# Kernel tuning notes

Hardware: AMD Instinct MI355X
Metric: run time of the kernel (lower is better)

Reference implementation:

```python
import jax, jax.numpy as jnp
import numpy as np

DS, TS = 2048, 4096          # drug_size, target_size
N = DS + TS                  # total nodes; also feature dim of x
E = 1048576                  # number of directed edges
NEG_SLOPE = 0.2              # PyG GATConv default negative_slope
GAMMA = 2.0 ** -5            # h1..h4 gamma
PS = [1.0, 0.5, 0.333, 0.25, 0.2]  # drug_ps == target_ps kernel weights


def _segment_softmax(logits, seg, n):
    # softmax over edges grouped by destination node (variable degree)
    m = jax.ops.segment_max(logits, seg, num_segments=n)
    m = jnp.where(jnp.isfinite(m), m, 0.0)
    e = jnp.exp(logits - m[seg])
    s = jax.ops.segment_sum(e, seg, num_segments=n)
    return e / s[seg]


def _gat(h, src, dst, W, a_src, a_dst, b, n):
    # PyG GATConv: linear -> per-edge attention logits -> segment softmax -> scatter-sum, concat heads
    Hh, F = a_src.shape
    z = (h @ W).reshape(n, Hh, F)          # [N, H, F]
    zs = z[src]                            # gather: [E, H, F]
    logit = jnp.einsum('ehf,hf->eh', zs, a_src) + jnp.einsum('ehf,hf->eh', z[dst], a_dst)
    alpha = _segment_softmax(jax.nn.leaky_relu(logit, NEG_SLOPE), dst, n)  # [E, H]
    out = jax.ops.segment_sum(alpha[:, :, None] * zs, dst, num_segments=n)  # scatter: [N, H, F]
    return out.reshape(n, Hh * F) + b


def _gip(y, gamma):
    # getGipKernel(y, 0, gamma, True): row min-max normalize, gram, scale by mean diag, gaussian of distance
    mn = y.min(axis=1, keepdims=True)
    mx = y.max(axis=1, keepdims=True)
    rng = mx - mn
    y = (y - mn) / jnp.where(rng == 0, 1.0, rng)
    k = y @ y.T
    k = k / jnp.mean(jnp.diagonal(k))
    d = jnp.diagonal(k)
    dist = d[:, None] + d[None, :] - 2.0 * k   # kernelToDistance
    return jnp.exp(-gamma * dist)


def _norm_kernel(K):
    # normalized_kernel: abs, replace zeros with min nonzero, divide by diag (D*D.T with 1-D D == diag(K))
    K = jnp.abs(K)
    minv = jnp.min(jnp.where(K == 0, jnp.inf, K))
    K = jnp.where(K == 0, minv, K)
    return K / jnp.diagonal(K)[None, :]


def setup_inputs() -> dict:
    key = jax.random.key(0)
    ks = jax.random.split(key, 24)

    def w(k, shape, fan_in):
        return jax.random.normal(k, shape, jnp.float32) / np.float32(np.sqrt(fan_in))

    return dict(
        x=jax.random.normal(ks[0], (N, N), jnp.float32),
        edge_index=jax.random.randint(ks[1], (2, E), 0, N, dtype=jnp.int32),
        W1=w(ks[2], (N, 256), N), a_src1=w(ks[3], (4, 64), 64), a_dst1=w(ks[4], (4, 64), 64), b1=jnp.zeros((256,), jnp.float32),
        W2=w(ks[5], (256, 256), 256), a_src2=w(ks[6], (4, 64), 64), a_dst2=w(ks[7], (4, 64), 64), b2=jnp.zeros((256,), jnp.float32),
        W3=w(ks[8], (256, 256), 256), a_src3=w(ks[9], (4, 64), 64), a_dst3=w(ks[10], (4, 64), 64), b3=jnp.zeros((256,), jnp.float32),
        W4=w(ks[11], (256, 128), 256), a_src4=w(ks[12], (4, 32), 32), a_dst4=w(ks[13], (4, 32), 32), b4=jnp.zeros((128,), jnp.float32),
        alpha1=jax.random.normal(ks[14], (DS, TS), jnp.float32),
        alpha2=jax.random.normal(ks[15], (TS, DS), jnp.float32),
        drug_sim=jax.random.uniform(ks[16], (DS, DS), jnp.float32),
        target_sim=jax.random.uniform(ks[17], (TS, TS), jnp.float32),
    )


def reference(x, edge_index, W1, a_src1, a_dst1, b1, W2, a_src2, a_dst2, b2,
              W3, a_src3, a_dst3, b3, W4, a_src4, a_dst4, b4,
              alpha1, alpha2, drug_sim, target_sim):
    n = x.shape[0]
    loop = jnp.arange(n, dtype=edge_index.dtype)   # GATConv add_self_loops=True
    src = jnp.concatenate([edge_index[0], loop])
    dst = jnp.concatenate([edge_index[1], loop])

    H1 = jax.nn.relu(_gat(x, src, dst, W1, a_src1, a_dst1, b1, n))
    H2 = jax.nn.relu(_gat(H1, src, dst, W2, a_src2, a_dst2, b2, n))
    H3 = jax.nn.relu(_gat(H2, src, dst, W3, a_src3, a_dst3, b3, n))
    H4 = jax.nn.relu(_gat(H3, src, dst, W4, a_src4, a_dst4, b4, n))

    dks = [_gip(H[:DS], GAMMA) for H in (H1, H2, H3, H4)] + [drug_sim]
    tks = [_gip(H[DS:], GAMMA) for H in (H1, H2, H3, H4)] + [target_sim]
    drug_k = sum(PS[i] * dks[i] for i in range(5))
    target_k = sum(PS[i] * tks[i] for i in range(5))
    drug_k = _norm_kernel(drug_k)
    target_k = _norm_kernel(target_k)

    out = (drug_k @ alpha1 + (target_k @ alpha2).T) / 2.0   # [DS, TS]
    return out
```

## Files before the change

kernel.cpp:

```cpp
#include <hip/hip_runtime.h>
#include <math.h>

#define NN 6144
#define DSZ 2048
#define TSZ 4096
#define NE 1048576
#define NE_TOT (NE + NN)
#define NEG_SLOPE 0.2f
#define GGAMMA 0.03125f

typedef float floatx4 __attribute__((ext_vector_type(4)));
typedef __bf16 bf16x8 __attribute__((ext_vector_type(8)));

__global__ void hist_kernel(const int* __restrict__ ei, int* __restrict__ cnt) {
    int e = blockIdx.x * blockDim.x + threadIdx.x;
    if (e >= NE_TOT) return;
    int d = (e < NE) ? ei[NE + e] : (e - NE);
    atomicAdd(&cnt[d], 1);
}

__global__ void scan_kernel(const int* __restrict__ cnt, int* __restrict__ row_ofs) {
    __shared__ int part[1024];
    int t = threadIdx.x;
    int local[6];
    int s = 0;
#pragma unroll
    for (int i = 0; i < 6; i++) { local[i] = s; s += cnt[t * 6 + i]; }
    part[t] = s;
    __syncthreads();
    for (int off = 1; off < 1024; off <<= 1) {
        int v = (t >= off) ? part[t - off] : 0;
        __syncthreads();
        part[t] += v;
        __syncthreads();
    }
    int base = (t == 0) ? 0 : part[t - 1];
#pragma unroll
    for (int i = 0; i < 6; i++) row_ofs[t * 6 + i] = base + local[i];
    if (t == 1023) row_ofs[NN] = part[1023];
}

__global__ void copy_cursor(const int* __restrict__ row_ofs, int* __restrict__ cursor) {
    int i = blockIdx.x * blockDim.x + threadIdx.x;
    if (i < NN) cursor[i] = row_ofs[i];
}

__global__ void scatter_kernel(const int* __restrict__ ei, int* __restrict__ cursor,
                               int* __restrict__ col) {
    int e = blockIdx.x * blockDim.x + threadIdx.x;
    if (e >= NE_TOT) return;
    int s, d;
    if (e < NE) { s = ei[e]; d = ei[NE + e]; } else { s = e - NE; d = s; }
    int pos = atomicAdd(&cursor[d], 1);
    col[pos] = s;
}

template <bool ATOMIC>
__global__ __launch_bounds__(256) void gemm64(const float* __restrict__ A,
                                              const float* __restrict__ B,
                                              float* __restrict__ C,
                                              int M, int N, int K) {
    __shared__ float As[16][68];
    __shared__ float Bs[16][68];
    const int tid = threadIdx.x;
    const int tn = tid & 15, tm = tid >> 4;
    const int bm = blockIdx.y * 64, bn = blockIdx.x * 64;
    const int ar = tid >> 2, ac = (tid & 3) * 4;
    const int br = tid >> 4, bc = (tid & 15) * 4;
    int kbeg = 0, kend = K;
    if constexpr (ATOMIC) {
        int klen = K / gridDim.z;
        kbeg = blockIdx.z * klen;
        kend = kbeg + klen;
    }
    const float* Ap = A + (size_t)(bm + ar) * K + ac;
    const float* Bp = B + (size_t)br * N + bn + bc;
    float acc[4][4] = {};
    for (int k0 = kbeg; k0 < kend; k0 += 16) {
        float4 av = *(const float4*)(Ap + k0);
        float4 bv = *(const float4*)(Bp + (size_t)k0 * N);
        As[ac + 0][ar] = av.x; As[ac + 1][ar] = av.y;
        As[ac + 2][ar] = av.z; As[ac + 3][ar] = av.w;
        *(float4*)&Bs[br][bc] = bv;
        __syncthreads();
#pragma unroll
        for (int k = 0; k < 16; k++) {
            float4 a4 = *(const float4*)&As[k][tm * 4];
            float4 b4 = *(const float4*)&Bs[k][tn * 4];
            float aa[4] = {a4.x, a4.y, a4.z, a4.w};
            float bb[4] = {b4.x, b4.y, b4.z, b4.w};
#pragma unroll
            for (int i = 0; i < 4; i++)
#pragma unroll
                for (int j = 0; j < 4; j++) acc[i][j] = fmaf(aa[i], bb[j], acc[i][j]);
        }
        __syncthreads();
    }
#pragma unroll
    for (int i = 0; i < 4; i++) {
        float* cp = C + (size_t)(bm + tm * 4 + i) * N + bn + tn * 4;
        if constexpr (ATOMIC) {
#pragma unroll
            for (int j = 0; j < 4; j++) atomicAdd(cp + j, acc[i][j]);
        } else {
            *(float4*)cp = make_float4(acc[i][0], acc[i][1], acc[i][2], acc[i][3]);
        }
    }
}

__device__ __forceinline__ ushort bf16_rne(float x) {
    unsigned u = __float_as_uint(x);
    unsigned r = (u + 0x7fffu + ((u >> 16) & 1u)) >> 16;
    return (ushort)r;
}

__global__ void split_rm(const float* __restrict__ in, ushort* __restrict__ hi,
                         ushort* __restrict__ lo, size_t n4) {
    for (size_t i = (size_t)blockIdx.x * blockDim.x + threadIdx.x; i < n4;
         i += (size_t)gridDim.x * blockDim.x) {
        float4 v = ((const float4*)in)[i];
        float vv[4] = {v.x, v.y, v.z, v.w};
        ushort h[4], l[4];
#pragma unroll
        for (int j = 0; j < 4; j++) {
            h[j] = bf16_rne(vv[j]);
            float hf = __uint_as_float((unsigned)h[j] << 16);
            l[j] = bf16_rne(vv[j] - hf);
        }
        ((ushort4*)hi)[i] = make_ushort4(h[0], h[1], h[2], h[3]);
        ((ushort4*)lo)[i] = make_ushort4(l[0], l[1], l[2], l[3]);
    }
}

__global__ void split_T(const float* __restrict__ in, ushort* __restrict__ hiT,
                        ushort* __restrict__ loT, int R, int C) {
    __shared__ float tile[32][33];
    int bx = blockIdx.x * 32, by = blockIdx.y * 32;
    int tx = threadIdx.x & 31, ty = threadIdx.x >> 5;
#pragma unroll
    for (int k = 0; k < 32; k += 8)
        tile[ty + k][tx] = in[(size_t)(by + ty + k) * C + bx + tx];
    __syncthreads();
#pragma unroll
    for (int k = 0; k < 32; k += 8) {
        float v = tile[tx][ty + k];
        ushort h = bf16_rne(v);
        float hf = __uint_as_float((unsigned)h << 16);
        ushort l = bf16_rne(v - hf);
        size_t o = (size_t)(bx + ty + k) * R + by + tx;
        hiT[o] = h;
        loT[o] = l;
    }
}

__device__ __forceinline__ void gl_lds16(const void* g, void* l) {
    __builtin_amdgcn_global_load_lds(
        (const __attribute__((address_space(1))) unsigned int*)g,
        (__attribute__((address_space(3))) unsigned int*)l, 16, 0, 0);
}

template <int EPI>
__global__ __launch_bounds__(256) void gemm_bt_x3(
    const ushort* __restrict__ Ah, const ushort* __restrict__ Al,
    const ushort* __restrict__ Bh, const ushort* __restrict__ Bl,
    float* __restrict__ C, int M, int N, int K,
    const float* __restrict__ rbuf, const float* __restrict__ md0buf, float p) {
    __shared__ ushort lds[4][4096];
    const int t = threadIdx.x;
    const int bm = blockIdx.y * 128, bn = blockIdx.x * 128;

    const int srow = t >> 2;
    const int scb = (t & 3) << 4;
    const int gcb = scb ^ (((srow >> 1) & 3) << 4);
    const int wid = t >> 6, lane = t & 63;

    const ushort* srcs[4] = {Ah, Al, Bh, Bl};
    const char* g[8];
    ushort* lp[8];
#pragma unroll
    for (int b = 0; b < 4; b++) {
        int rb = (b < 2) ? bm : bn;
#pragma unroll
        for (int i = 0; i < 2; i++) {
            g[b * 2 + i] = (const char*)srcs[b] + ((size_t)(rb + i * 64 + srow) * K) * 2 + gcb;
            lp[b * 2 + i] = &lds[b][i * 2048 + wid * 512];
        }
    }

    floatx4 acc[4][4];
#pragma unroll
    for (int m = 0; m < 4; m++)
#pragma unroll
        for (int n = 0; n < 4; n++) acc[m][n] = (floatx4){0.f, 0.f, 0.f, 0.f};

    const int wr = (wid >> 1) << 6, wc = (wid & 1) << 6;
    const int fr = lane & 15, kh = lane >> 4;
    const int cbf = (((kh << 4) ^ (((fr >> 1) & 3) << 4)) >> 1);

    for (int k0 = 0; k0 < K; k0 += 32) {
#pragma unroll
        for (int q = 0; q < 8; q++) gl_lds16(g[q] + (size_t)k0 * 2, lp[q]);
        __syncthreads();
        bf16x8 bhf[4], blf[4];
#pragma unroll
        for (int n = 0; n < 4; n++) {
            int r = wc + n * 16 + fr;
            bhf[n] = *(const bf16x8*)&lds[2][r * 32 + cbf];
            blf[n] = *(const bf16x8*)&lds[3][r * 32 + cbf];
        }
#pragma unroll
        for (int m = 0; m < 4; m++) {
            int r = wr + m * 16 + fr;
            bf16x8 ahf = *(const bf16x8*)&lds[0][r * 32 + cbf];
            bf16x8 alf = *(const bf16x8*)&lds[1][r * 32 + cbf];
#pragma unroll
            for (int n = 0; n < 4; n++) {
                acc[m][n] = __builtin_amdgcn_mfma_f32_16x16x32_bf16(ahf, bhf[n], acc[m][n], 0, 0, 0);
                acc[m][n] = __builtin_amdgcn_mfma_f32_16x16x32_bf16(ahf, blf[n], acc[m][n], 0, 0, 0);
                acc[m][n] = __builtin_amdgcn_mfma_f32_16x16x32_bf16(alf, bhf[n], acc[m][n], 0, 0, 0);
            }
        }
        __syncthreads();
    }

    float sc = 0.f;
    if constexpr (EPI == 1) sc = GGAMMA / md0buf[0];
#pragma unroll
    for (int m = 0; m < 4; m++) {
#pragma unroll
        for (int n = 0; n < 4; n++) {
#pragma unroll
            for (int r = 0; r < 4; r++) {
                int gr = bm + wr + m * 16 + kh * 4 + r;
                int gc = bn + wc + n * 16 + fr;
                size_t idx = (size_t)gr * N + gc;
                if constexpr (EPI == 0) {
                    C[idx] = acc[m][n][r];
                } else {
                    float val = p * expf(-(rbuf[gr] + rbuf[gc] - 2.f * acc[m][n][r]) * sc);
                    C[idx] += val;
                }
            }
        }
    }
}

__global__ void attn_scores(const float* __restrict__ z, const float* __restrict__ a_src,
                            const float* __restrict__ a_dst, float* __restrict__ s_src,
                            float* __restrict__ s_dst, int Fout, int F) {
    int n = blockIdx.x, t = threadIdx.x;
    __shared__ float r1[256], r2[256];
    float v = (t < Fout) ? z[(size_t)n * Fout + t] : 0.f;
    r1[t] = (t < Fout) ? v * a_src[t] : 0.f;
    r2[t] = (t < Fout) ? v * a_dst[t] : 0.f;
    __syncthreads();
    for (int off = F >> 1; off > 0; off >>= 1) {
        if ((t & (F - 1)) < off) { r1[t] += r1[t + off]; r2[t] += r2[t + off]; }
        __syncthreads();
    }
    if (t < Fout && (t & (F - 1)) == 0) {
        int h = t / F;
        s_src[n * 4 + h] = r1[t];
        s_dst[n * 4 + h] = r2[t];
    }
}

template <int FOUT, int F>
__global__ __launch_bounds__(256) void gat_aggregate(
    const float* __restrict__ z, const int* __restrict__ row_ofs,
    const int* __restrict__ col, const float* __restrict__ s_src,
    const float* __restrict__ s_dst, const float* __restrict__ bias,
    float* __restrict__ H) {
    constexpr int VPL = FOUT / 64;
    int wave = threadIdx.x >> 6, lane = threadIdx.x & 63;
    int n = blockIdx.x * 4 + wave;
    int beg = row_ofs[n], end = row_ofs[n + 1];
    int f0 = lane * VPL;
    int h = f0 / F;
    float4 sd4 = *(const float4*)&s_dst[n * 4];
    float mx[4] = {-__builtin_inff(), -__builtin_inff(), -__builtin_inff(), -__builtin_inff()};
    for (int e = beg + lane; e < end; e += 64) {
        int s = col[e];
        float4 ss = *(const float4*)&s_src[s * 4];
        float l0 = ss.x + sd4.x; l0 = l0 > 0.f ? l0 : NEG_SLOPE * l0;
        float l1 = ss.y + sd4.y; l1 = l1 > 0.f ? l1 : NEG_SLOPE * l1;
        float l2 = ss.z + sd4.z; l2 = l2 > 0.f ? l2 : NEG_SLOPE * l2;
        float l3 = ss.w + sd4.w; l3 = l3 > 0.f ? l3 : NEG_SLOPE * l3;
        mx[0] = fmaxf(mx[0], l0); mx[1] = fmaxf(mx[1], l1);
        mx[2] = fmaxf(mx[2], l2); mx[3] = fmaxf(mx[3], l3);
    }
#pragma unroll
    for (int off = 32; off > 0; off >>= 1) {
#pragma unroll
        for (int hh = 0; hh < 4; hh++) mx[hh] = fmaxf(mx[hh], __shfl_xor(mx[hh], off));
    }
    float mh = (h == 0) ? mx[0] : (h == 1) ? mx[1] : (h == 2) ? mx[2] : mx[3];
    float sdh = (h == 0) ? sd4.x : (h == 1) ? sd4.y : (h == 2) ? sd4.z : sd4.w;
    float acc[VPL] = {};
    float wsum = 0.f;
    for (int e = beg; e < end; e++) {
        int s = col[e];
        float l = s_src[s * 4 + h] + sdh;
        l = l > 0.f ? l : NEG_SLOPE * l;
        float w = expf(l - mh);
        wsum += w;
        const float* zp = z + (size_t)s * FOUT + f0;
        if constexpr (VPL == 4) {
            float4 zv = *(const float4*)zp;
            acc[0] = fmaf(w, zv.x, acc[0]); acc[1] = fmaf(w, zv.y, acc[1]);
            acc[2] = fmaf(w, zv.z, acc[2]); acc[3] = fmaf(w, zv.w, acc[3]);
        } else {
            float2 zv = *(const float2*)zp;
            acc[0] = fmaf(w, zv.x, acc[0]); acc[1] = fmaf(w, zv.y, acc[1]);
        }
    }
    float inv = 1.f / wsum;
#pragma unroll
    for (int i = 0; i < VPL; i++) {
        float o = acc[i] * inv + bias[f0 + i];
        H[(size_t)n * FOUT + f0 + i] = o > 0.f ? o : 0.f;
    }
}

__global__ void gip_norm(const float* __restrict__ Y, float* __restrict__ Yn,
                         float* __restrict__ r, int Fout) {
    int row = blockIdx.x, t = threadIdx.x;
    __shared__ float s1[256], s2[256];
    float v = Y[(size_t)row * Fout + t];
    s1[t] = v; s2[t] = v;
    __syncthreads();
    for (int off = blockDim.x >> 1; off > 0; off >>= 1) {
        if (t < off) {
            s1[t] = fminf(s1[t], s1[t + off]);
            s2[t] = fmaxf(s2[t], s2[t + off]);
        }
        __syncthreads();
    }
    float mn = s1[0], mx = s2[0];
    float rng = mx - mn;
    if (rng == 0.f) rng = 1.f;
    float yn = (v - mn) / rng;
    Yn[(size_t)row * Fout + t] = yn;
    __syncthreads();
    s1[t] = yn * yn;
    __syncthreads();
    for (int off = blockDim.x >> 1; off > 0; off >>= 1) {
        if (t < off) s1[t] += s1[t + off];
        __syncthreads();
    }
    if (t == 0) r[row] = s1[0];
}

__global__ void mean_reduce(const float* __restrict__ r, float* __restrict__ md0, int M) {
    __shared__ float s[1024];
    int t = threadIdx.x;
    float acc = 0.f;
    for (int i = t; i < M; i += 1024) acc += r[i];
    s[t] = acc;
    __syncthreads();
    for (int off = 512; off > 0; off >>= 1) {
        if (t < off) s[t] += s[t + off];
        __syncthreads();
    }
    if (t == 0) md0[0] = s[0] / (float)M;
}

__global__ __launch_bounds__(256) void gram64(const float* __restrict__ Y,
                                              float* __restrict__ Kacc,
                                              const float* __restrict__ rbuf,
                                              const float* __restrict__ md0buf,
                                              float p, int M, int K) {
    __shared__ float As[16][68];
    __shared__ float Bs[16][68];
    const int tid = threadIdx.x;
    const int tn = tid & 15, tm = tid >> 4;
    const int bm = blockIdx.y * 64, bn = blockIdx.x * 64;
    const int ar = tid >> 2, ac = (tid & 3) * 4;
    const float* Ap = Y + (size_t)(bm + ar) * K + ac;
    const float* Bp = Y + (size_t)(bn + ar) * K + ac;
    float acc[4][4] = {};
    for (int k0 = 0; k0 < K; k0 += 16) {
        float4 av = *(const float4*)(Ap + k0);
        float4 bv = *(const float4*)(Bp + k0);
        As[ac + 0][ar] = av.x; As[ac + 1][ar] = av.y;
        As[ac + 2][ar] = av.z; As[ac + 3][ar] = av.w;
        Bs[ac + 0][ar] = bv.x; Bs[ac + 1][ar] = bv.y;
        Bs[ac + 2][ar] = bv.z; Bs[ac + 3][ar] = bv.w;
        __syncthreads();
#pragma unroll
        for (int k = 0; k < 16; k++) {
            float4 a4 = *(const float4*)&As[k][tm * 4];
            float4 b4 = *(const float4*)&Bs[k][tn * 4];
            float aa[4] = {a4.x, a4.y, a4.z, a4.w};
            float bb[4] = {b4.x, b4.y, b4.z, b4.w};
#pragma unroll
            for (int i = 0; i < 4; i++)
#pragma unroll
                for (int j = 0; j < 4; j++) acc[i][j] = fmaf(aa[i], bb[j], acc[i][j]);
        }
        __syncthreads();
    }
    float sc = GGAMMA / md0buf[0];
    float ri[4], rj[4];
#pragma unroll
    for (int i = 0; i < 4; i++) ri[i] = rbuf[bm + tm * 4 + i];
#pragma unroll
    for (int j = 0; j < 4; j++) rj[j] = rbuf[bn + tn * 4 + j];
#pragma unroll
    for (int i = 0; i < 4; i++) {
#pragma unroll
        for (int j = 0; j < 4; j++) {
            float val = p * expf(-(ri[i] + rj[j] - 2.f * acc[i][j]) * sc);
            size_t idx = (size_t)(bm + tm * 4 + i) * M + bn + tn * 4 + j;
            Kacc[idx] += val;
        }
    }
}

__global__ void scale_copy(const float* __restrict__ src, float* __restrict__ dst,
                           float p, size_t n) {
    for (size_t i = (size_t)blockIdx.x * blockDim.x + threadIdx.x; i < n;
         i += (size_t)gridDim.x * blockDim.x)
        dst[i] = p * src[i];
}

__global__ void init_min(unsigned* minb) {
    if (threadIdx.x == 0 && blockIdx.x == 0) { minb[0] = 0x7f800000u; minb[1] = 0x7f800000u; }
}

__global__ void min_nonzero(const float* __restrict__ Km, unsigned* __restrict__ minb,
                            size_t total) {
    unsigned lm = 0x7f800000u;
    for (size_t i = (size_t)blockIdx.x * blockDim.x + threadIdx.x; i < total;
         i += (size_t)gridDim.x * blockDim.x) {
        float v = fabsf(Km[i]);
        if (v != 0.f) lm = min(lm, __float_as_uint(v));
    }
#pragma unroll
    for (int off = 32; off > 0; off >>= 1)
        lm = min(lm, (unsigned)__shfl_xor((int)lm, off));
    if ((threadIdx.x & 63) == 0) atomicMin(minb, lm);
}

__global__ void diag_abs(const float* __restrict__ Km, float* __restrict__ dbuf, int M) {
    int i = blockIdx.x * blockDim.x + threadIdx.x;
    if (i < M) dbuf[i] = fabsf(Km[(size_t)i * M + i]);
}

__global__ void normdiv(float* __restrict__ Km, const float* __restrict__ dbuf,
                        const unsigned* __restrict__ minb, int M) {
    int colc = blockIdx.x * blockDim.x + threadIdx.x;
    int row = blockIdx.y;
    float minv = __uint_as_float(minb[0]);
    float v = fabsf(Km[(size_t)row * M + colc]);
    if (v == 0.f) v = minv;
    float dj = dbuf[colc];
    if (dj == 0.f) dj = minv;
    Km[(size_t)row * M + colc] = v / dj;
}

__global__ void combine(float* __restrict__ out, const float* __restrict__ Bm) {
    __shared__ float t[32][33];
    int bx = blockIdx.x * 32;
    int by = blockIdx.y * 32;
    int tx = threadIdx.x & 31, ty = threadIdx.x >> 5;
#pragma unroll
    for (int k = 0; k < 32; k += 8)
        t[ty + k][tx] = Bm[(size_t)(bx + ty + k) * DSZ + by + tx];
    __syncthreads();
#pragma unroll
    for (int k = 0; k < 32; k += 8) {
        size_t idx = (size_t)(by + ty + k) * TSZ + bx + tx;
        out[idx] = 0.5f * (out[idx] + t[tx][ty + k]);
    }
}

extern "C" void kernel_launch(void* const* d_in, const int* in_sizes, int n_in,
                              void* d_out, int out_size, void* d_ws, size_t ws_size,
                              hipStream_t stream) {
    (void)in_sizes; (void)n_in; (void)out_size;
    const float* x      = (const float*)d_in[0];
    const int*   ei     = (const int*)d_in[1];
    const float* W1     = (const float*)d_in[2];
    const float* as1    = (const float*)d_in[3];
    const float* ad1    = (const float*)d_in[4];
    const float* b1     = (const float*)d_in[5];
    const float* W2     = (const float*)d_in[6];
    const float* as2    = (const float*)d_in[7];
    const float* ad2    = (const float*)d_in[8];
    const float* b2     = (const float*)d_in[9];
    const float* W3     = (const float*)d_in[10];
    const float* as3    = (const float*)d_in[11];
    const float* ad3    = (const float*)d_in[12];
    const float* b3     = (const float*)d_in[13];
    const float* W4     = (const float*)d_in[14];
    const float* as4    = (const float*)d_in[15];
    const float* ad4    = (const float*)d_in[16];
    const float* b4     = (const float*)d_in[17];
    const float* alpha1 = (const float*)d_in[18];
    const float* alpha2 = (const float*)d_in[19];
    const float* dsim   = (const float*)d_in[20];
    const float* tsim   = (const float*)d_in[21];
    float* out = (float*)d_out;

    char* base = (char*)d_ws;
    size_t off = 0;
    auto carve = [&](size_t bytes) -> void* {
        void* p = base + off;
        off = (off + bytes + 255) & ~(size_t)255;
        return p;
    };
    float* Bmat  = (float*)base;
    int* col     = (int*)carve((size_t)NE_TOT * 4);
    int* cnt     = (int*)carve((NN + 1) * 4);
    int* row_ofs = (int*)carve((NN + 1) * 4);
    int* cursor  = (int*)carve(NN * 4);
    float* s_src = (float*)carve((size_t)NN * 4 * 4);
    float* s_dst = (float*)carve((size_t)NN * 4 * 4);
    float* z     = (float*)carve((size_t)NN * 256 * 4);
    float* H1    = (float*)carve((size_t)NN * 256 * 4);
    float* H2    = (float*)carve((size_t)NN * 256 * 4);
    float* H3    = (float*)carve((size_t)NN * 256 * 4);
    float* H4    = (float*)carve((size_t)NN * 128 * 4);
    float* Yn    = (float*)carve((size_t)TSZ * 256 * 4);
    size_t bspan = ((size_t)TSZ * DSZ * 4 + 255) & ~(size_t)255;
    if (off < bspan) off = bspan;
    float* rbuf     = (float*)carve(TSZ * 4);
    float* md0      = (float*)carve(256);
    unsigned* minb  = (unsigned*)carve(256);
    float* dbD      = (float*)carve(DSZ * 4);
    float* dbT      = (float*)carve(TSZ * 4);
    float* drug_k   = (float*)carve((size_t)DSZ * DSZ * 4);
    float* tgt_k    = (float*)carve((size_t)TSZ * TSZ * 4);
    ushort* Ynh  = (ushort*)carve((size_t)TSZ * 256 * 2);
    ushort* Ynl  = (ushort*)carve((size_t)TSZ * 256 * 2);
    ushort* dkh  = (ushort*)carve((size_t)DSZ * DSZ * 2);
    ushort* dkl  = (ushort*)carve((size_t)DSZ * DSZ * 2);
    ushort* tkh  = (ushort*)carve((size_t)TSZ * TSZ * 2);
    ushort* tkl  = (ushort*)carve((size_t)TSZ * TSZ * 2);
    ushort* a1Th = (ushort*)carve((size_t)TSZ * DSZ * 2);
    ushort* a1Tl = (ushort*)carve((size_t)TSZ * DSZ * 2);
    ushort* a2Th = (ushort*)carve((size_t)DSZ * TSZ * 2);
    ushort* a2Tl = (ushort*)carve((size_t)DSZ * TSZ * 2);
    const bool use_mfma = (off <= ws_size);
    ushort* xh   = (ushort*)carve((size_t)NN * NN * 2);
    ushort* xl   = (ushort*)carve((size_t)NN * NN * 2);
    ushort* w1Th = (ushort*)carve((size_t)NN * 256 * 2);
    ushort* w1Tl = (ushort*)carve((size_t)NN * 256 * 2);
    const bool use_mfma_l1 = use_mfma && (off <= ws_size);

    hipMemsetAsync(cnt, 0, (NN + 1) * 4, stream);
    hist_kernel<<<(NE_TOT + 255) / 256, 256, 0, stream>>>(ei, cnt);
    scan_kernel<<<1, 1024, 0, stream>>>(cnt, row_ofs);
    copy_cursor<<<(NN + 255) / 256, 256, 0, stream>>>(row_ofs, cursor);
    scatter_kernel<<<(NE_TOT + 255) / 256, 256, 0, stream>>>(ei, cursor, col);

    if (use_mfma_l1) {
        split_rm<<<4096, 256, 0, stream>>>(x, xh, xl, (size_t)NN * NN / 4);
        split_T<<<dim3(256 / 32, NN / 32), 256, 0, stream>>>(W1, w1Th, w1Tl, NN, 256);
        gemm_bt_x3<0><<<dim3(256 / 128, NN / 128), 256, 0, stream>>>(
            xh, xl, w1Th, w1Tl, z, NN, 256, NN, rbuf, md0, 0.f);
    } else {
        hipMemsetAsync(z, 0, (size_t)NN * 256 * 4, stream);
        gemm64<true><<<dim3(256 / 64, NN / 64, 8), 256, 0, stream>>>(x, W1, z, NN, 256, NN);
    }
    attn_scores<<<NN, 256, 0, stream>>>(z, as1, ad1, s_src, s_dst, 256, 64);
    gat_aggregate<256, 64><<<NN / 4, 256, 0, stream>>>(z, row_ofs, col, s_src, s_dst, b1, H1);

    gemm64<false><<<dim3(256 / 64, NN / 64), 256, 0, stream>>>(H1, W2, z, NN, 256, 256);
    attn_scores<<<NN, 256, 0, stream>>>(z, as2, ad2, s_src, s_dst, 256, 64);
    gat_aggregate<256, 64><<<NN / 4, 256, 0, stream>>>(z, row_ofs, col, s_src, s_dst, b2, H2);

    gemm64<false><<<dim3(256 / 64, NN / 64), 256, 0, stream>>>(H2, W3, z, NN, 256, 256);
    attn_scores<<<NN, 256, 0, stream>>>(z, as3, ad3, s_src, s_dst, 256, 64);
    gat_aggregate<256, 64><<<NN / 4, 256, 0, stream>>>(z, row_ofs, col, s_src, s_dst, b3, H3);

    gemm64<false><<<dim3(128 / 64, NN / 64), 256, 0, stream>>>(H3, W4, z, NN, 128, 256);
    attn_scores<<<NN, 256, 0, stream>>>(z, as4, ad4, s_src, s_dst, 128, 32);
    gat_aggregate<128, 32><<<NN / 4, 256, 0, stream>>>(z, row_ofs, col, s_src, s_dst, b4, H4);

    scale_copy<<<4096, 256, 0, stream>>>(dsim, drug_k, 0.2f, (size_t)DSZ * DSZ);
    scale_copy<<<8192, 256, 0, stream>>>(tsim, tgt_k, 0.2f, (size_t)TSZ * TSZ);

    const float PSv[4] = {1.0f, 0.5f, 0.333f, 0.25f};
    const float* Hs[4] = {H1, H2, H3, H4};
    const int Fo[4] = {256, 256, 256, 128};
    for (int l = 0; l < 4; l++) {
        gip_norm<<<DSZ, Fo[l], 0, stream>>>(Hs[l], Yn, rbuf, Fo[l]);
        mean_reduce<<<1, 1024, 0, stream>>>(rbuf, md0, DSZ);
        if (use_mfma) {
            split_rm<<<2048, 256, 0, stream>>>(Yn, Ynh, Ynl, (size_t)DSZ * Fo[l] / 4);
            gemm_bt_x3<1><<<dim3(DSZ / 128, DSZ / 128), 256, 0, stream>>>(
                Ynh, Ynl, Ynh, Ynl, drug_k, DSZ, DSZ, Fo[l], rbuf, md0, PSv[l]);
        } else {
            gram64<<<dim3(DSZ / 64, DSZ / 64), 256, 0, stream>>>(Yn, drug_k, rbuf, md0,
                                                                 PSv[l], DSZ, Fo[l]);
        }
        gip_norm<<<TSZ, Fo[l], 0, stream>>>(Hs[l] + (size_t)DSZ * Fo[l], Yn, rbuf, Fo[l]);
        mean_reduce<<<1, 1024, 0, stream>>>(rbuf, md0, TSZ);
        if (use_mfma) {
            split_rm<<<2048, 256, 0, stream>>>(Yn, Ynh, Ynl, (size_t)TSZ * Fo[l] / 4);
            gemm_bt_x3<1><<<dim3(TSZ / 128, TSZ / 128), 256, 0, stream>>>(
                Ynh, Ynl, Ynh, Ynl, tgt_k, TSZ, TSZ, Fo[l], rbuf, md0, PSv[l]);
        } else {
            gram64<<<dim3(TSZ / 64, TSZ / 64), 256, 0, stream>>>(Yn, tgt_k, rbuf, md0,
                                                                 PSv[l], TSZ, Fo[l]);
        }
    }

    init_min<<<1, 64, 0, stream>>>(minb);
    min_nonzero<<<1024, 256, 0, stream>>>(drug_k, minb + 0, (size_t)DSZ * DSZ);
    diag_abs<<<(DSZ + 255) / 256, 256, 0, stream>>>(drug_k, dbD, DSZ);
    normdiv<<<dim3(DSZ / 256, DSZ), 256, 0, stream>>>(drug_k, dbD, minb + 0, DSZ);
    min_nonzero<<<1024, 256, 0, stream>>>(tgt_k, minb + 1, (size_t)TSZ * TSZ);
    diag_abs<<<(TSZ + 255) / 256, 256, 0, stream>>>(tgt_k, dbT, TSZ);
    normdiv<<<dim3(TSZ / 256, TSZ), 256, 0, stream>>>(tgt_k, dbT, minb + 1, TSZ);

    if (use_mfma) {
        split_T<<<dim3(TSZ / 32, DSZ / 32), 256, 0, stream>>>(alpha1, a1Th, a1Tl, DSZ, TSZ);
        split_T<<<dim3(DSZ / 32, TSZ / 32), 256, 0, stream>>>(alpha2, a2Th, a2Tl, TSZ, DSZ);
        split_rm<<<2048, 256, 0, stream>>>(drug_k, dkh, dkl, (size_t)DSZ * DSZ / 4);
        split_rm<<<2048, 256, 0, stream>>>(tgt_k, tkh, tkl, (size_t)TSZ * TSZ / 4);
        gemm_bt_x3<0><<<dim3(TSZ / 128, DSZ / 128), 256, 0, stream>>>(
            dkh, dkl, a1Th, a1Tl, out, DSZ, TSZ, DSZ, rbuf, md0, 0.f);
        gemm_bt_x3<0><<<dim3(DSZ / 128, TSZ / 128), 256, 0, stream>>>(
            tkh, tkl, a2Th, a2Tl, Bmat, TSZ, DSZ, TSZ, rbuf, md0, 0.f);
    } else {
        gemm64<false><<<dim3(TSZ / 64, DSZ / 64), 256, 0, stream>>>(drug_k, alpha1, out,
                                                                    DSZ, TSZ, DSZ);
        gemm64<false><<<dim3(DSZ / 64, TSZ / 64), 256, 0, stream>>>(tgt_k, alpha2, Bmat,
                                                                    TSZ, DSZ, TSZ);
    }
    combine<<<dim3(TSZ / 32, DSZ / 32), 256, 0, stream>>>(out, Bmat);
}
```

Before: 2.311 ms.

## Fuse GIP grams across layers, split-K first GEMM, MFMA for small GAT GEMMs

```diff
diff --git a/kernel.cpp b/kernel.cpp
--- a/kernel.cpp
+++ b/kernel.cpp
@@ -8,6 +8,7 @@
 #define NE_TOT (NE + NN)
 #define NEG_SLOPE 0.2f
 #define GGAMMA 0.03125f
+#define LDCAT 896
 
 typedef float floatx4 __attribute__((ext_vector_type(4)));
 typedef __bf16 bf16x8 __attribute__((ext_vector_type(8)));
@@ -163,8 +164,7 @@
 __global__ __launch_bounds__(256) void gemm_bt_x3(
     const ushort* __restrict__ Ah, const ushort* __restrict__ Al,
     const ushort* __restrict__ Bh, const ushort* __restrict__ Bl,
-    float* __restrict__ C, int M, int N, int K,
-    const float* __restrict__ rbuf, const float* __restrict__ md0buf, float p) {
+    float* __restrict__ C, int M, int N, int K) {
     __shared__ ushort lds[4][4096];
     const int t = threadIdx.x;
     const int bm = blockIdx.y * 128, bn = blockIdx.x * 128;
@@ -174,6 +174,13 @@
     const int gcb = scb ^ (((srow >> 1) & 3) << 4);
     const int wid = t >> 6, lane = t & 63;
 
+    int kbeg = 0, kend = K;
+    if (gridDim.z > 1) {
+        int klen = K / gridDim.z;
+        kbeg = blockIdx.z * klen;
+        kend = kbeg + klen;
+    }
+
     const ushort* srcs[4] = {Ah, Al, Bh, Bl};
     const char* g[8];
     ushort* lp[8];
@@ -197,7 +204,7 @@
     const int fr = lane & 15, kh = lane >> 4;
     const int cbf = (((kh << 4) ^ (((fr >> 1) & 3) << 4)) >> 1);
 
-    for (int k0 = 0; k0 < K; k0 += 32) {
+    for (int k0 = kbeg; k0 < kend; k0 += 32) {
 #pragma unroll
         for (int q = 0; q < 8; q++) gl_lds16(g[q] + (size_t)k0 * 2, lp[q]);
         __syncthreads();
@@ -223,8 +230,6 @@
         __syncthreads();
     }
 
-    float sc = 0.f;
-    if constexpr (EPI == 1) sc = GGAMMA / md0buf[0];
 #pragma unroll
     for (int m = 0; m < 4; m++) {
 #pragma unroll
@@ -234,12 +239,112 @@
                 int gr = bm + wr + m * 16 + kh * 4 + r;
                 int gc = bn + wc + n * 16 + fr;
                 size_t idx = (size_t)gr * N + gc;
-                if constexpr (EPI == 0) {
-                    C[idx] = acc[m][n][r];
-                } else {
-                    float val = p * expf(-(rbuf[gr] + rbuf[gc] - 2.f * acc[m][n][r]) * sc);
-                    C[idx] += val;
+                if constexpr (EPI == 0) C[idx] = acc[m][n][r];
+                else atomicAdd(&C[idx], acc[m][n][r]);
+            }
+        }
+    }
+}
+
+__global__ __launch_bounds__(256) void gram_fused(
+    const ushort* __restrict__ Yh, const ushort* __restrict__ Yl,
+    const float* __restrict__ sim, float* __restrict__ Kout,
+    const float* __restrict__ rbufs,
+    const float* __restrict__ md0s,
+    int M) {
+    __shared__ ushort lds[4][4096];
+    const int t = threadIdx.x;
+    const int bm = blockIdx.y * 128, bn = blockIdx.x * 128;
+    const int srow = t >> 2;
+    const int scb = (t & 3) << 4;
+    const int gcb = scb ^ (((srow >> 1) & 3) << 4);
+    const int wid = t >> 6, lane = t & 63;
+
+    const ushort* srcs[4] = {Yh, Yl, Yh, Yl};
+    const char* g[8];
+    ushort* lp[8];
+#pragma unroll
+    for (int b = 0; b < 4; b++) {
+        int rb = (b < 2) ? bm : bn;
+#pragma unroll
+        for (int i = 0; i < 2; i++) {
+            g[b * 2 + i] = (const char*)srcs[b] + ((size_t)(rb + i * 64 + srow) * LDCAT) * 2 + gcb;
+            lp[b * 2 + i] = &lds[b][i * 2048 + wid * 512];
+        }
+    }
+
+    const int wr = (wid >> 1) << 6, wc = (wid & 1) << 6;
+    const int fr = lane & 15, kh = lane >> 4;
+    const int cbf = (((kh << 4) ^ (((fr >> 1) & 3) << 4)) >> 1);
+
+    floatx4 epi[4][4];
+#pragma unroll
+    for (int m = 0; m < 4; m++)
+#pragma unroll
+        for (int n = 0; n < 4; n++) epi[m][n] = (floatx4){0.f, 0.f, 0.f, 0.f};
+
+#pragma unroll
+    for (int l = 0; l < 4; l++) {
+        const int kofs = l * 256;
+        const int klen = (l == 3) ? 128 : 256;
+        const float pl = (l == 0) ? 1.0f : (l == 1) ? 0.5f : (l == 2) ? 0.333f : 0.25f;
+        floatx4 acc[4][4];
+#pragma unroll
+        for (int m = 0; m < 4; m++)
+#pragma unroll
+            for (int n = 0; n < 4; n++) acc[m][n] = (floatx4){0.f, 0.f, 0.f, 0.f};
+#pragma unroll 1
+        for (int k0 = kofs; k0 < kofs + klen; k0 += 32) {
+#pragma unroll
+            for (int q = 0; q < 8; q++) gl_lds16(g[q] + (size_t)k0 * 2, lp[q]);
+            __syncthreads();
+            bf16x8 bhf[4], blf[4];
+#pragma unroll
+            for (int n = 0; n < 4; n++) {
+                int r = wc + n * 16 + fr;
+                bhf[n] = *(const bf16x8*)&lds[2][r * 32 + cbf];
+                blf[n] = *(const bf16x8*)&lds[3][r * 32 + cbf];
+            }
+#pragma unroll
+            for (int m = 0; m < 4; m++) {
+                int r = wr + m * 16 + fr;
+                bf16x8 ahf = *(const bf16x8*)&lds[0][r * 32 + cbf];
+                bf16x8 alf = *(const bf16x8*)&lds[1][r * 32 + cbf];
+#pragma unroll
+                for (int n = 0; n < 4; n++) {
+                    acc[m][n] = __builtin_amdgcn_mfma_f32_16x16x32_bf16(ahf, bhf[n], acc[m][n], 0, 0, 0);
+                    acc[m][n] = __builtin_amdgcn_mfma_f32_16x16x32_bf16(ahf, blf[n], acc[m][n], 0, 0, 0);
+                    acc[m][n] = __builtin_amdgcn_mfma_f32_16x16x32_bf16(alf, bhf[n], acc[m][n], 0, 0, 0);
                 }
+            }
+            __syncthreads();
+        }
+        float sc = GGAMMA / md0s[l];
+        const float* rb_ = rbufs + (size_t)l * M;
+#pragma unroll
+        for (int m = 0; m < 4; m++) {
+#pragma unroll
+            for (int r = 0; r < 4; r++) {
+                float ri = rb_[bm + wr + m * 16 + kh * 4 + r];
+#pragma unroll
+                for (int n = 0; n < 4; n++) {
+                    float rj = rb_[bn + wc + n * 16 + fr];
+                    epi[m][n][r] += pl * expf(-(ri + rj - 2.f * acc[m][n][r]) * sc);
+                }
+            }
+        }
+    }
+
+#pragma unroll
+    for (int m = 0; m < 4; m++) {
+#pragma unroll
+        for (int n = 0; n < 4; n++) {
+#pragma unroll
+            for (int r = 0; r < 4; r++) {
+                int gr = bm + wr + m * 16 + kh * 4 + r;
+                int gc = bn + wc + n * 16 + fr;
+                size_t idx = (size_t)gr * M + gc;
+                Kout[idx] = 0.2f * sim[idx] + epi[m][n][r];
             }
         }
     }
@@ -322,6 +427,45 @@
     }
 }
 
+__global__ void gip_norm_split(const float* __restrict__ Y, ushort* __restrict__ Yh,
+                               ushort* __restrict__ Yl, float* __restrict__ r,
+                               float* __restrict__ md0p, float invM,
+                               int Fout, int kofs) {
+    int row = blockIdx.x, t = threadIdx.x;
+    __shared__ float s1[256], s2[256];
+    float v = Y[(size_t)row * Fout + t];
+    s1[t] = v; s2[t] = v;
+    __syncthreads();
+    for (int off = blockDim.x >> 1; off > 0; off >>= 1) {
+        if (t < off) {
+            s1[t] = fminf(s1[t], s1[t + off]);
+            s2[t] = fmaxf(s2[t], s2[t + off]);
+        }
+        __syncthreads();
+    }
+    float mn = s1[0], mx = s2[0];
+    float rng = mx - mn;
+    if (rng == 0.f) rng = 1.f;
+    float yn = (v - mn) / rng;
+    ushort h = bf16_rne(yn);
+    float hf = __uint_as_float((unsigned)h << 16);
+    ushort lo = bf16_rne(yn - hf);
+    size_t o = (size_t)row * LDCAT + kofs + t;
+    Yh[o] = h;
+    Yl[o] = lo;
+    __syncthreads();
+    s1[t] = yn * yn;
+    __syncthreads();
+    for (int off = blockDim.x >> 1; off > 0; off >>= 1) {
+        if (t < off) s1[t] += s1[t + off];
+        __syncthreads();
+    }
+    if (t == 0) {
+        r[row] = s1[0];
+        atomicAdd(md0p, s1[0] * invM);
+    }
+}
+
 __global__ void gip_norm(const float* __restrict__ Y, float* __restrict__ Yn,
                          float* __restrict__ r, int Fout) {
     int row = blockIdx.x, t = threadIdx.x;
@@ -445,6 +589,24 @@
 __global__ void diag_abs(const float* __restrict__ Km, float* __restrict__ dbuf, int M) {
     int i = blockIdx.x * blockDim.x + threadIdx.x;
     if (i < M) dbuf[i] = fabsf(Km[(size_t)i * M + i]);
+}
+
+__global__ void normdiv_split(const float* __restrict__ Km, const float* __restrict__ dbuf,
+                              const unsigned* __restrict__ minb,
+                              ushort* __restrict__ kh, ushort* __restrict__ kl, int M) {
+    int colc = blockIdx.x * blockDim.x + threadIdx.x;
+    int row = blockIdx.y;
+    float minv = __uint_as_float(minb[0]);
+    float v = fabsf(Km[(size_t)row * M + colc]);
+    if (v == 0.f) v = minv;
+    float dj = dbuf[colc];
+    if (dj == 0.f) dj = minv;
+    float rr = v / dj;
+    ushort h = bf16_rne(rr);
+    float hf = __uint_as_float((unsigned)h << 16);
+    size_t o = (size_t)row * M + colc;
+    kh[o] = h;
+    kl[o] = bf16_rne(rr - hf);
 }
 
 __global__ void normdiv(float* __restrict__ Km, const float* __restrict__ dbuf,
@@ -522,32 +684,39 @@
     float* H2    = (float*)carve((size_t)NN * 256 * 4);
     float* H3    = (float*)carve((size_t)NN * 256 * 4);
     float* H4    = (float*)carve((size_t)NN * 128 * 4);
-    float* Yn    = (float*)carve((size_t)TSZ * 256 * 4);
+    float* Yn_fb = (float*)carve((size_t)TSZ * 256 * 4);
     size_t bspan = ((size_t)TSZ * DSZ * 4 + 255) & ~(size_t)255;
     if (off < bspan) off = bspan;
-    float* rbuf     = (float*)carve(TSZ * 4);
-    float* md0      = (float*)carve(256);
+    float* rbD      = (float*)carve((size_t)4 * DSZ * 4);
+    float* rbT      = (float*)carve((size_t)4 * TSZ * 4);
+    float* md0D     = (float*)carve(256);
+    float* md0T     = (float*)carve(256);
     unsigned* minb  = (unsigned*)carve(256);
     float* dbD      = (float*)carve(DSZ * 4);
     float* dbT      = (float*)carve(TSZ * 4);
     float* drug_k   = (float*)carve((size_t)DSZ * DSZ * 4);
     float* tgt_k    = (float*)carve((size_t)TSZ * TSZ * 4);
-    ushort* Ynh  = (ushort*)carve((size_t)TSZ * 256 * 2);
-    ushort* Ynl  = (ushort*)carve((size_t)TSZ * 256 * 2);
-    ushort* dkh  = (ushort*)carve((size_t)DSZ * DSZ * 2);
-    ushort* dkl  = (ushort*)carve((size_t)DSZ * DSZ * 2);
-    ushort* tkh  = (ushort*)carve((size_t)TSZ * TSZ * 2);
-    ushort* tkl  = (ushort*)carve((size_t)TSZ * TSZ * 2);
+    ushort* YdH  = (ushort*)carve((size_t)DSZ * LDCAT * 2);
+    ushort* YdL  = (ushort*)carve((size_t)DSZ * LDCAT * 2);
+    ushort* YtH  = (ushort*)carve((size_t)TSZ * LDCAT * 2);
+    ushort* YtL  = (ushort*)carve((size_t)TSZ * LDCAT * 2);
     ushort* a1Th = (ushort*)carve((size_t)TSZ * DSZ * 2);
     ushort* a1Tl = (ushort*)carve((size_t)TSZ * DSZ * 2);
     ushort* a2Th = (ushort*)carve((size_t)DSZ * TSZ * 2);
     ushort* a2Tl = (ushort*)carve((size_t)DSZ * TSZ * 2);
-    const bool use_mfma = (off <= ws_size);
+    ushort* Hh   = (ushort*)carve((size_t)NN * 256 * 2);
+    ushort* Hl   = (ushort*)carve((size_t)NN * 256 * 2);
+    ushort* wTh  = (ushort*)carve((size_t)256 * 256 * 2);
+    ushort* wTl  = (ushort*)carve((size_t)256 * 256 * 2);
     ushort* xh   = (ushort*)carve((size_t)NN * NN * 2);
     ushort* xl   = (ushort*)carve((size_t)NN * NN * 2);
     ushort* w1Th = (ushort*)carve((size_t)NN * 256 * 2);
     ushort* w1Tl = (ushort*)carve((size_t)NN * 256 * 2);
-    const bool use_mfma_l1 = use_mfma && (off <= ws_size);
+    const bool use_mfma = (off <= ws_size);
+    ushort* dkh = xh;
+    ushort* dkl = dkh + (size_t)DSZ * DSZ;
+    ushort* tkh = dkl + (size_t)DSZ * DSZ;
+    ushort* tkl = tkh + (size_t)TSZ * TSZ;
 
     hipMemsetAsync(cnt, 0, (NN + 1) * 4, stream);
     hist_kernel<<<(NE_TOT + 255) / 256, 256, 0, stream>>>(ei, cnt);
@@ -555,77 +724,103 @@
     copy_cursor<<<(NN + 255) / 256, 256, 0, stream>>>(row_ofs, cursor);
     scatter_kernel<<<(NE_TOT + 255) / 256, 256, 0, stream>>>(ei, cursor, col);
 
-    if (use_mfma_l1) {
+    const float PSv[4] = {1.0f, 0.5f, 0.333f, 0.25f};
+    float* Hs[4] = {H1, H2, H3, H4};
+    const int Fo[4] = {256, 256, 256, 128};
+
+    if (use_mfma) {
         split_rm<<<4096, 256, 0, stream>>>(x, xh, xl, (size_t)NN * NN / 4);
         split_T<<<dim3(256 / 32, NN / 32), 256, 0, stream>>>(W1, w1Th, w1Tl, NN, 256);
-        gemm_bt_x3<0><<<dim3(256 / 128, NN / 128), 256, 0, stream>>>(
-            xh, xl, w1Th, w1Tl, z, NN, 256, NN, rbuf, md0, 0.f);
+        hipMemsetAsync(z, 0, (size_t)NN * 256 * 4, stream);
+        gemm_bt_x3<2><<<dim3(2, NN / 128, 8), 256, 0, stream>>>(xh, xl, w1Th, w1Tl, z,
+                                                                NN, 256, NN);
+        attn_scores<<<NN, 256, 0, stream>>>(z, as1, ad1, s_src, s_dst, 256, 64);
+        gat_aggregate<256, 64><<<NN / 4, 256, 0, stream>>>(z, row_ofs, col, s_src, s_dst, b1, H1);
+
+        const float* Ws[3] = {W2, W3, W4};
+        const float* ass[3] = {as2, as3, as4};
+        const float* ads[3] = {ad2, ad3, ad4};
+        const float* bs[3] = {b2, b3, b4};
+        for (int l = 0; l < 3; l++) {
+            int Nout = (l == 2) ? 128 : 256;
+            split_rm<<<1024, 256, 0, stream>>>(Hs[l], Hh, Hl, (size_t)NN * 256 / 4);
+            split_T<<<dim3(Nout / 32, 256 / 32), 256, 0, stream>>>(Ws[l], wTh, wTl, 256, Nout);
+            hipMemsetAsync(z, 0, (size_t)NN * Nout * 4, stream);
+            gemm_bt_x3<2><<<dim3(Nout / 128, NN / 128, 2), 256, 0, stream>>>(
+                Hh, Hl, wTh, wTl, z, NN, Nout, 256);
+            attn_scores<<<NN, 256, 0, stream>>>(z, ass[l], ads[l], s_src, s_dst, Nout, Nout / 4);
+            if (l < 2)
+                gat_aggregate<256, 64><<<NN / 4, 256, 0, stream>>>(z, row_ofs, col, s_src,
+                                                                   s_dst, bs[l], Hs[l + 1]);
+            else
+                gat_aggregate<128, 32><<<NN / 4, 256, 0, stream>>>(z, row_ofs, col, s_src,
+                                                                   s_dst, bs[l], Hs[l + 1]);
+        }
+
+        hipMemsetAsync(md0D, 0, 256, stream);
+        hipMemsetAsync(md0T, 0, 256, stream);
+        for (int l = 0; l < 4; l++) {
+            gip_norm_split<<<DSZ, Fo[l], 0, stream>>>(Hs[l], YdH, YdL, rbD + l * DSZ,
+                                                      md0D + l, 1.f / DSZ, Fo[l], l * 256);
+            gip_norm_split<<<TSZ, Fo[l], 0, stream>>>(Hs[l] + (size_t)DSZ * Fo[l], YtH, YtL,
+                                                      rbT + l * TSZ, md0T + l, 1.f / TSZ,
+                                                      Fo[l], l * 256);
+        }
+        gram_fused<<<dim3(DSZ / 128, DSZ / 128), 256, 0, stream>>>(YdH, YdL, dsim, drug_k,
+                                                                   rbD, md0D, DSZ);
+        gram_fused<<<dim3(TSZ / 128, TSZ / 128), 256, 0, stream>>>(YtH, YtL, tsim, tgt_k,
+                                                                   rbT, md0T, TSZ);
+
+        init_min<<<1, 64, 0, stream>>>(minb);
+        min_nonzero<<<1024, 256, 0, stream>>>(drug_k, minb + 0, (size_t)DSZ * DSZ);
+        diag_abs<<<(DSZ + 255) / 256, 256, 0, stream>>>(drug_k, dbD, DSZ);
+        normdiv_split<<<dim3(DSZ / 256, DSZ), 256, 0, stream>>>(drug_k, dbD, minb + 0,
+                                                                dkh, dkl, DSZ);
+        min_nonzero<<<1024, 256, 0, stream>>>(tgt_k, minb + 1, (size_t)TSZ * TSZ);
+        diag_abs<<<(TSZ + 255) / 256, 256, 0, stream>>>(tgt_k, dbT, TSZ);
+        normdiv_split<<<dim3(TSZ / 256, TSZ), 256, 0, stream>>>(tgt_k, dbT, minb + 1,
+                                                                tkh, tkl, TSZ);
+
+        split_T<<<dim3(TSZ / 32, DSZ / 32), 256, 0, stream>>>(alpha1, a1Th, a1Tl, DSZ, TSZ);
+        split_T<<<dim3(DSZ / 32, TSZ / 32), 256, 0, stream>>>(alpha2, a2Th, a2Tl, TSZ, DSZ);
+        gemm_bt_x3<0><<<dim3(TSZ / 128, DSZ / 128), 256, 0, stream>>>(dkh, dkl, a1Th, a1Tl,
+                                                                      out, DSZ, TSZ, DSZ);
+        gemm_bt_x3<0><<<dim3(DSZ / 128, TSZ / 128), 256, 0, stream>>>(tkh, tkl, a2Th, a2Tl,
+                                                                      Bmat, TSZ, DSZ, TSZ);
     } else {
         hipMemsetAsync(z, 0, (size_t)NN * 256 * 4, stream);
         gemm64<true><<<dim3(256 / 64, NN / 64, 8), 256, 0, stream>>>(x, W1, z, NN, 256, NN);
-    }
-    attn_scores<<<NN, 256, 0, stream>>>(z, as1, ad1, s_src, s_dst, 256, 64);
-    gat_aggregate<256, 64><<<NN / 4, 256, 0, stream>>>(z, row_ofs, col, s_src, s_dst, b1, H1);
-
-    gemm64<false><<<dim3(256 / 64, NN / 64), 256, 0, stream>>>(H1, W2, z, NN, 256, 256);
-    attn_scores<<<NN, 256, 0, stream>>>(z, as2, ad2, s_src, s_dst, 256, 64);
-    gat_aggregate<256, 64><<<NN / 4, 256, 0, stream>>>(z, row_ofs, col, s_src, s_dst, b2, H2);
-
-    gemm64<false><<<dim3(256 / 64, NN / 64), 256, 0, stream>>>(H2, W3, z, NN, 256, 256);
-    attn_scores<<<NN, 256, 0, stream>>>(z, as3, ad3, s_src, s_dst, 256, 64);
-    gat_aggregate<256, 64><<<NN / 4, 256, 0, stream>>>(z, row_ofs, col, s_src, s_dst, b3, H3);
-
-    gemm64<false><<<dim3(128 / 64, NN / 64), 256, 0, stream>>>(H3, W4, z, NN, 128, 256);
-    attn_scores<<<NN, 256, 0, stream>>>(z, as4, ad4, s_src, s_dst, 128, 32);
-    gat_aggregate<128, 32><<<NN / 4, 256, 0, stream>>>(z, row_ofs, col, s_src, s_dst, b4, H4);
-
-    scale_copy<<<4096, 256, 0, stream>>>(dsim, drug_k, 0.2f, (size_t)DSZ * DSZ);
-    scale_copy<<<8192, 256, 0, stream>>>(tsim, tgt_k, 0.2f, (size_t)TSZ * TSZ);
-
-    const float PSv[4] = {1.0f, 0.5f, 0.333f, 0.25f};
-    const float* Hs[4] = {H1, H2, H3, H4};
-    const int Fo[4] = {256, 256, 256, 128};
-    for (int l = 0; l < 4; l++) {
-        gip_norm<<<DSZ, Fo[l], 0, stream>>>(Hs[l], Yn, rbuf, Fo[l]);
-        mean_reduce<<<1, 1024, 0, stream>>>(rbuf, md0, DSZ);
-        if (use_mfma) {
-            split_rm<<<2048, 256, 0, stream>>>(Yn, Ynh, Ynl, (size_t)DSZ * Fo[l] / 4);
-            gemm_bt_x3<1><<<dim3(DSZ / 128, DSZ / 128), 256, 0, stream>>>(
-                Ynh, Ynl, Ynh, Ynl, drug_k, DSZ, DSZ, Fo[l], rbuf, md0, PSv[l]);
-        } else {
-            gram64<<<dim3(DSZ / 64, DSZ / 64), 256, 0, stream>>>(Yn, drug_k, rbuf, md0,
+        attn_scores<<<NN, 256, 0, stream>>>(z, as1, ad1, s_src, s_dst, 256, 64);
+        gat_aggregate<256, 64><<<NN / 4, 256, 0, stream>>>(z, row_ofs, col, s_src, s_dst, b1, H1);
+        gemm64<false><<<dim3(256 / 64, NN / 64), 256, 0, stream>>>(H1, W2, z, NN, 256, 256);
+        attn_scores<<<NN, 256, 0, stream>>>(z, as2, ad2, s_src, s_dst, 256, 64);
+        gat_aggregate<256, 64><<<NN / 4, 256, 0, stream>>>(z, row_ofs, col, s_src, s_dst, b2, H2);
+        gemm64<false><<<dim3(256 / 64, NN / 64), 256, 0, stream>>>(H2, W3, z, NN, 256, 256);
+        attn_scores<<<NN, 256, 0, stream>>>(z, as3, ad3, s_src, s_dst, 256, 64);
+        gat_aggregate<256, 64><<<NN / 4, 256, 0, stream>>>(z, row_ofs, col, s_src, s_dst, b3, H3);
+        gemm64<false><<<dim3(128 / 64, NN / 64), 256, 0, stream>>>(H3, W4, z, NN, 128, 256);
+        attn_scores<<<NN, 256, 0, stream>>>(z, as4, ad4, s_src, s_dst, 128, 32);
+        gat_aggregate<128, 32><<<NN / 4, 256, 0, stream>>>(z, row_ofs, col, s_src, s_dst, b4, H4);
+
+        scale_copy<<<4096, 256, 0, stream>>>(dsim, drug_k, 0.2f, (size_t)DSZ * DSZ);
+        scale_copy<<<8192, 256, 0, stream>>>(tsim, tgt_k, 0.2f, (size_t)TSZ * TSZ);
+        for (int l = 0; l < 4; l++) {
+            gip_norm<<<DSZ, Fo[l], 0, stream>>>(Hs[l], Yn_fb, rbT, Fo[l]);
+            mean_reduce<<<1, 1024, 0, stream>>>(rbT, md0T, DSZ);
+            gram64<<<dim3(DSZ / 64, DSZ / 64), 256, 0, stream>>>(Yn_fb, drug_k, rbT, md0T,
                                                                  PSv[l], DSZ, Fo[l]);
-        }
-        gip_norm<<<TSZ, Fo[l], 0, stream>>>(Hs[l] + (size_t)DSZ * Fo[l], Yn, rbuf, Fo[l]);
-        mean_reduce<<<1, 1024, 0, stream>>>(rbuf, md0, TSZ);
-        if (use_mfma) {
-            split_rm<<<2048, 256, 0, stream>>>(Yn, Ynh, Ynl, (size_t)TSZ * Fo[l] / 4);
-            gemm_bt_x3<1><<<dim3(TSZ / 128, TSZ / 128), 256, 0, stream>>>(
-                Ynh, Ynl, Ynh, Ynl, tgt_k, TSZ, TSZ, Fo[l], rbuf, md0, PSv[l]);
-        } else {
-            gram64<<<dim3(TSZ / 64, TSZ / 64), 256, 0, stream>>>(Yn, tgt_k, rbuf, md0,
+            gip_norm<<<TSZ, Fo[l], 0, stream>>>(Hs[l] + (size_t)DSZ * Fo[l], Yn_fb, rbT, Fo[l]);
+            mean_reduce<<<1, 1024, 0, stream>>>(rbT, md0T, TSZ);
+            gram64<<<dim3(TSZ / 64, TSZ / 64), 256, 0, stream>>>(Yn_fb, tgt_k, rbT, md0T,
                                                                  PSv[l], TSZ, Fo[l]);
         }
-    }
-
-    init_min<<<1, 64, 0, stream>>>(minb);
-    min_nonzero<<<1024, 256, 0, stream>>>(drug_k, minb + 0, (size_t)DSZ * DSZ);
-    diag_abs<<<(DSZ + 255) / 256, 256, 0, stream>>>(drug_k, dbD, DSZ);
-    normdiv<<<dim3(DSZ / 256, DSZ), 256, 0, stream>>>(drug_k, dbD, minb + 0, DSZ);
-    min_nonzero<<<1024, 256, 0, stream>>>(tgt_k, minb + 1, (size_t)TSZ * TSZ);
-    diag_abs<<<(TSZ + 255) / 256, 256, 0, stream>>>(tgt_k, dbT, TSZ);
-    normdiv<<<dim3(TSZ / 256, TSZ), 256, 0, stream>>>(tgt_k, dbT, minb + 1, TSZ);
-
-    if (use_mfma) {
-        split_T<<<dim3(TSZ / 32, DSZ / 32), 256, 0, stream>>>(alpha1, a1Th, a1Tl, DSZ, TSZ);
-        split_T<<<dim3(DSZ / 32, TSZ / 32), 256, 0, stream>>>(alpha2, a2Th, a2Tl, TSZ, DSZ);
-        split_rm<<<2048, 256, 0, stream>>>(drug_k, dkh, dkl, (size_t)DSZ * DSZ / 4);
-        split_rm<<<2048, 256, 0, stream>>>(tgt_k, tkh, tkl, (size_t)TSZ * TSZ / 4);
-        gemm_bt_x3<0><<<dim3(TSZ / 128, DSZ / 128), 256, 0, stream>>>(
-            dkh, dkl, a1Th, a1Tl, out, DSZ, TSZ, DSZ, rbuf, md0, 0.f);
-        gemm_bt_x3<0><<<dim3(DSZ / 128, TSZ / 128), 256, 0, stream>>>(
-            tkh, tkl, a2Th, a2Tl, Bmat, TSZ, DSZ, TSZ, rbuf, md0, 0.f);
-    } else {
+        init_min<<<1, 64, 0, stream>>>(minb);
+        min_nonzero<<<1024, 256, 0, stream>>>(drug_k, minb + 0, (size_t)DSZ * DSZ);
+        diag_abs<<<(DSZ + 255) / 256, 256, 0, stream>>>(drug_k, dbD, DSZ);
+        normdiv<<<dim3(DSZ / 256, DSZ), 256, 0, stream>>>(drug_k, dbD, minb + 0, DSZ);
+        min_nonzero<<<1024, 256, 0, stream>>>(tgt_k, minb + 1, (size_t)TSZ * TSZ);
+        diag_abs<<<(TSZ + 255) / 256, 256, 0, stream>>>(tgt_k, dbT, TSZ);
+        normdiv<<<dim3(TSZ / 256, TSZ), 256, 0, stream>>>(tgt_k, dbT, minb + 1, TSZ);
         gemm64<false><<<dim3(TSZ / 64, DSZ / 64), 256, 0, stream>>>(drug_k, alpha1, out,
                                                                     DSZ, TSZ, DSZ);
         gemm64<false><<<dim3(DSZ / 64, TSZ / 64), 256, 0, stream>>>(tgt_k, alpha2, Bmat,
```

New measurement: 2.356 ms. About the same (+2.0%).
